# Performance work log

Hardware: AMD Instinct MI355X
Metric: run time of the kernel (lower is better)

## Reference

```python
import jax, jax.numpy as jnp
import numpy as np

PATCH = 64
STRIDE = PATCH // 2
SEQ = 65536
NPATCH = (SEQ - PATCH) // STRIDE + 1  # 2047
B = 256
EPS = 1e-5


def setup_inputs() -> dict:
    key = jax.random.key(0)
    ks = jax.random.split(key, 10)
    s = lambda k, shp: jax.random.normal(k, shp, jnp.float32) * 0.05
    return dict(
        x=jax.random.normal(ks[0], (B, 1, SEQ), jnp.float32),
        conv1_w=s(ks[1], (NPATCH, NPATCH - 1)),
        conv1_b=s(ks[2], (NPATCH,)),
        w1=s(ks[3], (32, 3, 5)), b1=s(ks[4], (32,)),
        g1=jnp.ones((32,), jnp.float32), be1=jnp.zeros((32,), jnp.float32),
        w2=s(ks[5], (64, 32, 3)), b2=s(ks[6], (64,)),
        g2=jnp.ones((64,), jnp.float32), be2=jnp.zeros((64,), jnp.float32),
        w3=s(ks[7], (128, 64, 3)), b3=s(ks[8], (128,)),
        g3=jnp.ones((128,), jnp.float32), be3=jnp.zeros((128,), jnp.float32),
    )


def _conv1d(x, w, b, pad):
    # x: [B, Cin, L], w: [Cout, Cin, K]
    y = jax.lax.conv_general_dilated(x, w, (1,), [(pad, pad)],
                                     dimension_numbers=('NCH', 'OIH', 'NCH'))
    return y + b[None, :, None]


def _bn(x, g, be):
    # training-mode BatchNorm1d: biased var over (batch, length)
    m = jnp.mean(x, axis=(0, 2), keepdims=True)
    v = jnp.var(x, axis=(0, 2), keepdims=True)
    return (x - m) * jax.lax.rsqrt(v + EPS) * g[None, :, None] + be[None, :, None]


def _maxpool2(x):
    # MaxPool1d(kernel=2, stride=2), floor division of length
    L = x.shape[-1] // 2
    return x[..., : 2 * L].reshape(x.shape[0], x.shape[1], L, 2).max(-1)


def reference(x, conv1_w, conv1_b, w1, b1, g1, be1, w2, b2, g2, be2, w3, b3, g3, be3):
    starts = jnp.arange(NPATCH) * STRIDE
    idx = starts[:, None] + jnp.arange(PATCH)[None, :]         # [NW, W]
    xp = x[:, :, idx]                                          # [B,1,NW,W]
    mean = xp.mean(-1)                                         # [B,1,NW]
    std = jnp.std(xp, axis=-1, ddof=1)                         # torch.std is unbiased
    stats = jnp.concatenate([mean, std], axis=1)               # [B,2,NW]
    dx = jnp.diff(xp, axis=2)                                  # diff across window index: [B,1,NW-1,W]
    dmax = dx.max(-1)                                          # [B,1,NW-1]
    dmax = jnp.transpose(dmax, (0, 2, 1))                      # [B,NW-1,1]
    # conv1: 1x1 Conv1d over length-1 axis == matmul over channel dim
    d2 = jnp.einsum('oi,bil->bol', conv1_w, dmax) + conv1_b[None, :, None]  # [B,NW,1]
    d2 = jnp.transpose(d2, (0, 2, 1))                          # [B,1,NW]
    x3 = jnp.concatenate([stats, d2], axis=1)                  # [B,3,NW]
    h = _maxpool2(jax.nn.relu(_bn(_conv1d(x3, w1, b1, 2), g1, be1)))
    h = _maxpool2(jax.nn.relu(_bn(_conv1d(h, w2, b2, 1), g2, be2)))
    h = jax.nn.relu(_bn(_conv1d(h, w3, b3, 1), g3, be3))
    return h.mean(-1)                                          # AdaptiveAvgPool1d(1)+Flatten -> [B,128]
```

## Files before the change

### kernel.cpp

```cpp
#include <hip/hip_runtime.h>
#include <math.h>

#define NB 256
#define SEQ 65536
#define NP 2047
#define NPM 2046
#define NPP 2048
#define KPAD 2048
#define LEN1 2047
#define LEN2 1023
#define LEN3 511
#define C1 32
#define C2 64
#define C3 128
#define NPART 2048
#define NPART2 (NB*4)
#define LPAD 514
#define SROW 40

#define OFF_X3   0
#define SZ_X3    (NB*3*NPP)
#define OFF_DMAX (OFF_X3 + SZ_X3)
#define SZ_DMAX  (NB*NPM)
#define OFF_Y1   (OFF_DMAX + SZ_DMAX)
#define SZ_Y1    (NB*C1*LEN1)
#define OFF_Y2   (OFF_Y1 + SZ_Y1)
#define SZ_Y2    (NB*C2*LEN2)
#define OFF_S1   (OFF_Y2 + SZ_Y2)
#define OFF_S2   (OFF_S1 + 2*C1)
#define OFF_S3   (OFF_S2 + 2*C2)
#define OFF_W2C  (OFF_S3 + 2*C3)
#define OFF_W3B  (OFF_W2C + C1*C2*3)
#define OFF_PS   (OFF_W3B + C2*C3*3)
#define OFF_PQ   (OFF_PS + C3*NPART)
#define OFF_WB   OFF_Y2
#define OFF_H1R  OFF_Y2
#define OFF_H2T  OFF_Y2
#define OFF_PM   (OFF_Y1 + 4300000)
#define OFF_W2B  OFF_W2C

typedef __attribute__((ext_vector_type(8))) short short8;
typedef __attribute__((ext_vector_type(4))) short short4v;
typedef __attribute__((ext_vector_type(4))) float f32x4;

__device__ inline short f2bf(float f){
  union { float f; unsigned u; } x; x.f = f;
  unsigned r = x.u + 0x7FFF + ((x.u >> 16) & 1);
  return (short)(r >> 16);
}

#define RED4L(v) v += __shfl_xor(v,1,64); v += __shfl_xor(v,2,64); \
                 v += __shfl_xor(v,4,64); v += __shfl_xor(v,8,64);

#define TILES(X) X(0,0) X(0,1) X(0,2) X(0,3) X(1,0) X(1,1) X(1,2) X(1,3) \
                 X(2,0) X(2,1) X(2,2) X(2,3) X(3,0) X(3,1) X(3,2) X(3,3)
#define DECLBIAS(P,ct) f32x4 bi##ct = *(const f32x4*)((P) + cbase + ct*16 + kq*4);
#define DECLACC(lt,ct) f32x4 acc##lt##ct = bi##ct;

__global__ __launch_bounds__(256) void k_patch(const float* __restrict__ x, const float* __restrict__ c1b,
                                               float* __restrict__ ws){
  float* x3    = ws + OFF_X3;
  short* dmaxB = (short*)(ws + OFF_DMAX);
  int b = blockIdx.y;
  int chunk = blockIdx.x;
  const float* xr = x + (size_t)b*SEQ + chunk*2048;
  __shared__ float Ss[65], Qs[65], Dm[65];
  int w = threadIdx.x >> 6;
  int l = threadIdx.x & 63;
  #pragma unroll
  for (int i=0;i<2;i++){
    int seg = w*2 + i;
    int off = seg*256;
    float4 A = *(const float4*)(xr + off + l*4);
    float4 Bh = make_float4(0.f,0.f,0.f,0.f);
    if (l >= 56){
      int g = chunk*2048 + off + 256 + (l-56)*4;
      if (g + 3 < SEQ) Bh = *(const float4*)(xr + off + 256 + (l-56)*4);
    }
    int src = (l+8) & 63;
    float p0 = __shfl(A.x, src, 64), p1 = __shfl(A.y, src, 64),
          p2 = __shfl(A.z, src, 64), p3 = __shfl(A.w, src, 64);
    if (l >= 56){ p0=Bh.x; p1=Bh.y; p2=Bh.z; p3=Bh.w; }
    float s = (A.x+A.y)+(A.z+A.w);
    float q = fmaf(A.x,A.x, fmaf(A.y,A.y, fmaf(A.z,A.z, A.w*A.w)));
    float d = fmaxf(fmaxf(p0-A.x, p1-A.y), fmaxf(p2-A.z, p3-A.w));
    #pragma unroll
    for (int o=1;o<8;o<<=1){
      s += __shfl_xor(s,o,64);
      q += __shfl_xor(q,o,64);
      d  = fmaxf(d, __shfl_xor(d,o,64));
    }
    if ((l&7)==0){ int m = seg*8 + (l>>3); Ss[m]=s; Qs[m]=q; Dm[m]=d; }
  }
  if (w==0){
    float s=0.f,q=0.f,d=-1e30f;
    if (l < 8){
      int g = chunk*2048 + 2048 + l*4;
      if (g+3 < SEQ){
        float4 A = *(const float4*)(xr + 2048 + l*4);
        float4 P = make_float4(0.f,0.f,0.f,0.f);
        if (g+35 < SEQ) P = *(const float4*)(xr + 2048 + 32 + l*4);
        s = (A.x+A.y)+(A.z+A.w);
        q = fmaf(A.x,A.x, fmaf(A.y,A.y, fmaf(A.z,A.z, A.w*A.w)));
        d = fmaxf(fmaxf(P.x-A.x, P.y-A.y), fmaxf(P.z-A.z, P.w-A.w));
      }
    }
    #pragma unroll
    for (int o=1;o<8;o<<=1){
      s += __shfl_xor(s,o,64);
      q += __shfl_xor(q,o,64);
      d  = fmaxf(d, __shfl_xor(d,o,64));
    }
    if (l==0){ Ss[64]=s; Qs[64]=q; Dm[64]=d; }
  }
  __syncthreads();
  if (threadIdx.x < 64){
    int j = threadIdx.x;
    int p = chunk*64 + j;
    if (p < NP){
      float S = Ss[j]+Ss[j+1];
      float Q = Qs[j]+Qs[j+1];
      float mean = S*(1.0f/64.0f);
      float var  = (Q - S*mean)*(1.0f/63.0f);
      x3[(size_t)(b*3+0)*NPP + p] = mean;
      x3[(size_t)(b*3+1)*NPP + p] = sqrtf(fmaxf(var,0.0f));
      x3[(size_t)(b*3+2)*NPP + p] = c1b[p];
    }
    dmaxB[(size_t)b*KPAD + p] = (p < NPM) ? f2bf(fmaxf(Dm[j], Dm[j+1])) : (short)0;
  }
}

__global__ __launch_bounds__(256) void k_prep(const float* __restrict__ W, const float* __restrict__ w2,
                                              const float* __restrict__ w3, float* __restrict__ ws){
  int bid = blockIdx.x;
  if (bid < 8*NP){
    short* Wb = (short*)(ws + OFF_WB);
    int o = bid >> 3;
    int k = (bid & 7)*256 + threadIdx.x;
    Wb[(size_t)o*KPAD + k] = (k < NPM) ? f2bf(W[(size_t)o*NPM + k]) : (short)0;
  } else {
    short* w2b = (short*)(ws + OFF_W2B);
    short* w3b = (short*)(ws + OFF_W3B);
    int t = (bid - 8*NP)*256 + threadIdx.x;
    if (t < 3*C2*C1){
      int tap = t / (C2*C1);
      int r = t - tap*(C2*C1);
      int c = r >> 5, i = r & 31;
      w2b[t] = f2bf(w2[(c*C1 + i)*3 + tap]);
    }
    if (t < 3*C3*C2){
      int tap = t / (C3*C2);
      int r = t - tap*(C3*C2);
      int c = r / C2, i = r - c*C2;
      w3b[(tap*C3 + c)*C2 + i] = f2bf(w3[(c*C2+i)*3 + tap]);
    }
  }
}

__global__ __launch_bounds__(256) void k_gemm(float* __restrict__ ws){
  const short* Ab = (const short*)(ws + OFF_DMAX);
  const short* Bb = (const short*)(ws + OFF_WB);
  float* x3 = ws + OFF_X3;
  int wid  = __builtin_amdgcn_readfirstlane(threadIdx.x >> 6);
  int lane = threadIdx.x & 63;
  int ln = lane & 15, kq = lane >> 4;
  int n0  = blockIdx.x*32;
  int m16 = (blockIdx.y*4 + wid)*16;
  int ks  = blockIdx.z*512;
  f32x4 acc0 = {0.f,0.f,0.f,0.f}, acc1 = {0.f,0.f,0.f,0.f};
  int o0 = n0 + ln, o1 = n0 + 16 + ln;
  const short* ap  = Ab + (size_t)(m16 + ln)*KPAD + ks + kq*8;
  const short* bp0 = Bb + (size_t)min(o0, NP-1)*KPAD + ks + kq*8;
  const short* bp1 = Bb + (size_t)min(o1, NP-1)*KPAD + ks + kq*8;
  #pragma unroll 4
  for (int s=0; s<16; s++){
    short8 av = *(const short8*)(ap  + s*32);
    short8 b0 = *(const short8*)(bp0 + s*32);
    short8 b1 = *(const short8*)(bp1 + s*32);
    acc0 = __builtin_amdgcn_mfma_f32_16x16x32_bf16(av, b0, acc0, 0, 0, 0);
    acc1 = __builtin_amdgcn_mfma_f32_16x16x32_bf16(av, b1, acc1, 0, 0, 0);
  }
  #pragma unroll
  for (int r=0;r<4;r++){
    int b = m16 + kq*4 + r;
    float* xp = x3 + ((size_t)(b*3) + 2)*NPP;
    if (o0 < NP) atomicAdd(xp + o0, acc0[r]);
    if (o1 < NP) atomicAdd(xp + o1, acc1[r]);
  }
}

__global__ __launch_bounds__(256) void k_conv1f(const float* __restrict__ w1, const float* __restrict__ b1, float* __restrict__ ws){
  const float* x3 = ws + OFF_X3;
  float* h1r = ws + OFF_H1R;
  float* ps = ws + OFF_PS;
  float* pq = ws + OFF_PQ;
  int b = blockIdx.y;
  int blk = blockIdx.x;
  int w = threadIdx.x >> 6;
  int lane = threadIdx.x & 63;
  int h = lane >> 5, c = lane & 31;
  int p0 = blk*256 + w*64 + h*32;
  float wv[3][5];
  #pragma unroll
  for (int i=0;i<3;i++){
    #pragma unroll
    for (int j=0;j<5;j++) wv[i][j] = w1[(c*3+i)*5+j];
  }
  float bc = b1[c];
  const float* xb = x3 + (size_t)b*3*NPP;
  float s = 0.f, q = 0.f;
  #pragma unroll
  for (int k0=0;k0<32;k0+=8){
    int base = p0 + k0 - 4;
    float xw[3][16];
    #pragma unroll
    for (int i=0;i<3;i++){
      const float* xr = xb + (size_t)i*NPP;
      if (base >= 0 && base + 16 <= LEN1){
        #pragma unroll
        for (int t=0;t<4;t++) *(f32x4*)&xw[i][4*t] = *(const f32x4*)(xr + base + 4*t);
      } else {
        #pragma unroll
        for (int t=0;t<16;t++){ int g = base + t; xw[i][t] = (g >= 0 && g < LEN1) ? xr[g] : 0.f; }
      }
    }
    float acc[8];
    #pragma unroll
    for (int k=0;k<8;k++){
      float a = bc;
      #pragma unroll
      for (int i=0;i<3;i++){
        #pragma unroll
        for (int j=0;j<5;j++) a = fmaf(wv[i][j], xw[i][k+j+2], a);
      }
      acc[k] = a;
      if (p0 + k0 + k < LEN1){ s += a; q = fmaf(a, a, q); }
    }
    #pragma unroll
    for (int t=0;t<4;t++){
      int m = ((p0 + k0) >> 1) + t;
      if (m < LEN2) h1r[((size_t)b*LEN2 + m)*C1 + c] = fmaxf(acc[2*t], acc[2*t+1]);
    }
  }
  s += __shfl_xor(s, 32, 64);
  q += __shfl_xor(q, 32, 64);
  __shared__ float es[4][C1], eq[4][C1];
  if (h == 0){ es[w][c] = s; eq[w][c] = q; }
  __syncthreads();
  if (threadIdx.x < C1){
    int cc = threadIdx.x;
    float S = es[0][cc]+es[1][cc]+es[2][cc]+es[3][cc];
    float Q = eq[0][cc]+eq[1][cc]+eq[2][cc]+eq[3][cc];
    ps[(size_t)cc*NPART + b*8 + blk] = S;
    pq[(size_t)cc*NPART + b*8 + blk] = Q;
  }
}

__global__ __launch_bounds__(256) void k_fin(const float* __restrict__ ps, const float* __restrict__ pq,
                                             const float* __restrict__ g, const float* __restrict__ be,
                                             float* __restrict__ stats, int C, int npart, double invN,
                                             float* __restrict__ outz){
  if (outz) outz[(size_t)threadIdx.x * C3 + blockIdx.x] = 0.f;
  int c = blockIdx.x;
  double s=0.0, q=0.0;
  for (int j=threadIdx.x; j<npart; j+=256){ s += (double)ps[c*npart+j]; q += (double)pq[c*npart+j]; }
  #pragma unroll
  for (int off=32; off; off>>=1){ s += __shfl_xor(s,off,64); q += __shfl_xor(q,off,64); }
  __shared__ double rs[4], rq[4];
  int wid = threadIdx.x>>6, lane=threadIdx.x&63;
  if (lane==0){ rs[wid]=s; rq[wid]=q; }
  __syncthreads();
  if (threadIdx.x==0){
    double S = rs[0]+rs[1]+rs[2]+rs[3];
    double Q = rq[0]+rq[1]+rq[2]+rq[3];
    double mean = S*invN;
    double var  = Q*invN - mean*mean;
    double a = (double)g[c] / sqrt(var + 1e-5);
    stats[c]   = (float)a;
    stats[C+c] = (float)((double)be[c] - mean*a);
  }
}

__global__ __launch_bounds__(256) void k_conv2m(const float* __restrict__ b2, float* __restrict__ ws){
  const float* h1r = ws + OFF_H1R;
  const float* st1 = ws + OFF_S1;
  const short* w2b = (const short*)(ws + OFF_W2B);
  float* pmaxT = ws + OFF_PM;
  float* ps = ws + OFF_PS;
  float* pq = ws + OFF_PQ;
  int b   = blockIdx.y;
  int blk = blockIdx.x;
  int l0  = blk*256;
  __shared__ __align__(16) short sh[258*SROW];
  for (int u = threadIdx.x; u < 258*8; u += 256){
    int row = u >> 3, g = u & 7;
    int pos = l0 - 1 + row;
    short4v r4 = (short4v)0;
    if (pos >= 0 && pos < LEN2){
      f32x4 xv = *(const f32x4*)(h1r + ((size_t)b*LEN2 + pos)*C1 + g*4);
      f32x4 av = *(const f32x4*)(st1 + g*4);
      f32x4 bb = *(const f32x4*)(st1 + C1 + g*4);
      #pragma unroll
      for (int j=0;j<4;j++) r4[j] = f2bf(fmaxf(fmaf(av[j], xv[j], bb[j]), 0.f));
    }
    *(short4v*)(sh + row*SROW + g*4) = r4;
  }
  __syncthreads();
  int w   = __builtin_amdgcn_readfirstlane(threadIdx.x >> 6);
  int lane = threadIdx.x & 63;
  int ln = lane & 15, kq = lane >> 4;
  int lw = l0 + w*64;
  int cbase = 0;
  DECLBIAS(b2,0) DECLBIAS(b2,1) DECLBIAS(b2,2) DECLBIAS(b2,3)
  TILES(DECLACC)
  const short* wA = w2b + (size_t)ln*C1 + kq*8;
#define LDW(T,ct) short8 aw##T##ct = *(const short8*)(wA + (size_t)(T*C2 + ct*16)*C1);
  LDW(0,0) LDW(0,1) LDW(0,2) LDW(0,3)
  LDW(1,0) LDW(1,1) LDW(1,2) LDW(1,3)
  LDW(2,0) LDW(2,1) LDW(2,2) LDW(2,3)
#undef LDW
#define MMT0(lt,ct) acc##lt##ct = __builtin_amdgcn_mfma_f32_16x16x32_bf16(aw0##ct, bv##lt, acc##lt##ct, 0, 0, 0);
#define MMT1(lt,ct) acc##lt##ct = __builtin_amdgcn_mfma_f32_16x16x32_bf16(aw1##ct, bv##lt, acc##lt##ct, 0, 0, 0);
#define MMT2(lt,ct) acc##lt##ct = __builtin_amdgcn_mfma_f32_16x16x32_bf16(aw2##ct, bv##lt, acc##lt##ct, 0, 0, 0);
#define LDB2(lt,T) short8 bv##lt = *(const short8*)(sh + (size_t)(w*64 + lt*16 + T + ln)*SROW + kq*8);
#define CSTEP(T) { LDB2(0,T) LDB2(1,T) LDB2(2,T) LDB2(3,T) TILES(MMT##T) }
  CSTEP(0) CSTEP(1) CSTEP(2)
#undef CSTEP
#undef LDB2
#define PST(lt,ct) { \
    float p0_ = fmaxf(acc##lt##ct[0], __shfl_xor(acc##lt##ct[0],1,64)); \
    float p1_ = fmaxf(acc##lt##ct[1], __shfl_xor(acc##lt##ct[1],1,64)); \
    float p2_ = fmaxf(acc##lt##ct[2], __shfl_xor(acc##lt##ct[2],1,64)); \
    float p3_ = fmaxf(acc##lt##ct[3], __shfl_xor(acc##lt##ct[3],1,64)); \
    int l_ = lw + lt*16 + ln; \
    if (!(ln & 1) && (l_ >> 1) < LEN3){ \
      f32x4 pv_ = {p0_, p1_, p2_, p3_}; \
      *(f32x4*)(pmaxT + ((size_t)b*LEN3 + (l_>>1))*C2 + ct*16 + kq*4) = pv_; } }
  TILES(PST)
#undef PST
  __shared__ float es[4][C2], eq[4][C2];
  #pragma unroll
  for (int ct=0;ct<4;ct++){
    float s0=0.f,s1=0.f,s2=0.f,s3=0.f,q0=0.f,q1=0.f,q2=0.f,q3=0.f;
#define ACCST(lt,CT) if (CT == ct){ int l_ = lw + lt*16 + ln; if (l_ < LEN2){ \
      s0 += acc##lt##CT[0]; q0 = fmaf(acc##lt##CT[0], acc##lt##CT[0], q0); \
      s1 += acc##lt##CT[1]; q1 = fmaf(acc##lt##CT[1], acc##lt##CT[1], q1); \
      s2 += acc##lt##CT[2]; q2 = fmaf(acc##lt##CT[2], acc##lt##CT[2], q2); \
      s3 += acc##lt##CT[3]; q3 = fmaf(acc##lt##CT[3], acc##lt##CT[3], q3); } }
    TILES(ACCST)
#undef ACCST
    RED4L(s0) RED4L(s1) RED4L(s2) RED4L(s3)
    RED4L(q0) RED4L(q1) RED4L(q2) RED4L(q3)
    if (ln == 0){
      int c0 = ct*16 + kq*4;
      es[w][c0+0]=s0; es[w][c0+1]=s1; es[w][c0+2]=s2; es[w][c0+3]=s3;
      eq[w][c0+0]=q0; eq[w][c0+1]=q1; eq[w][c0+2]=q2; eq[w][c0+3]=q3;
    }
  }
  __syncthreads();
  if (threadIdx.x < C2){
    int c = threadIdx.x;
    float S = es[0][c]+es[1][c]+es[2][c]+es[3][c];
    float Q = eq[0][c]+eq[1][c]+eq[2][c]+eq[3][c];
    ps[(size_t)c*NPART2 + b*4 + blk] = S;
    pq[(size_t)c*NPART2 + b*4 + blk] = Q;
  }
}

__global__ __launch_bounds__(256) void k_p2bf(float* __restrict__ ws){
  const float* pm = ws + OFF_PM;
  const float* st = ws + OFF_S2;
  short* h2t = (short*)(ws + OFF_H2T);
  int b = blockIdx.y;
  int idx = blockIdx.x*256 + threadIdx.x;
  if (idx < LEN3*C2){
    int m = idx >> 6, c = idx & 63;
    float v = fmaxf(fmaf(st[c], pm[((size_t)b*LEN3 + m)*C2 + c], st[C2+c]), 0.f);
    h2t[(((size_t)b*8 + (c>>3))*LPAD + m + 1)*8 + (c&7)] = f2bf(v);
  } else {
    int zr = idx - LEN3*C2;
    if (zr < 3*C2){
      int rsel = zr >> 6, c = zr & 63;
      int row = (rsel == 0) ? 0 : (511 + rsel);
      h2t[(((size_t)b*8 + (c>>3))*LPAD + row)*8 + (c&7)] = 0;
    }
  }
}

__global__ __launch_bounds__(256) void k_conv3s(const float* __restrict__ b3, float* __restrict__ ws){
  const short* h2t = (const short*)(ws + OFF_H2T);
  const short* w3b = (const short*)(ws + OFF_W3B);
  float* ps = ws + OFF_PS;
  float* pq = ws + OFF_PQ;
  int b   = blockIdx.y;
  int blk = blockIdx.x;
  int wid = __builtin_amdgcn_readfirstlane(threadIdx.x >> 6);
  int lane = threadIdx.x & 63;
  int ln = lane & 15, kq = lane >> 4;
  int lh = wid & 1, ch = wid >> 1;
  int l0 = blk*128 + lh*64;
  int cbase = ch*64;
  DECLBIAS(b3,0) DECLBIAS(b3,1) DECLBIAS(b3,2) DECLBIAS(b3,3)
  TILES(DECLACC)
  const short* hB = h2t + (((size_t)b*8 + kq)*LPAD + l0 + ln)*8;
  const short* wA = w3b + (size_t)(cbase + ln)*C2 + kq*8;
  #pragma unroll
  for (int t=0;t<3;t++){
    #pragma unroll
    for (int s=0;s<2;s++){
#define LDB(lt) short8 bv##lt = *(const short8*)(hB + ((size_t)s*4*LPAD + lt*16 + t)*8);
      LDB(0) LDB(1) LDB(2) LDB(3)
#define LDA(ct) short8 av##ct = *(const short8*)(wA + (size_t)(t*C3 + ct*16)*C2 + s*32);
      LDA(0) LDA(1) LDA(2) LDA(3)
#define MM(lt,ct) acc##lt##ct = __builtin_amdgcn_mfma_f32_16x16x32_bf16(av##ct, bv##lt, acc##lt##ct, 0, 0, 0);
      TILES(MM)
#undef LDB
#undef LDA
    }
  }
  int pidx = b*8 + blk*2 + lh;
  #pragma unroll
  for (int ct=0;ct<4;ct++){
    float s0=0.f,s1=0.f,s2=0.f,s3=0.f,q0=0.f,q1=0.f,q2=0.f,q3=0.f;
#define ACCST(lt,CT) if (CT == ct){ int l_ = l0 + lt*16 + ln; if (l_ < LEN3){ \
      s0 += acc##lt##CT[0]; q0 = fmaf(acc##lt##CT[0], acc##lt##CT[0], q0); \
      s1 += acc##lt##CT[1]; q1 = fmaf(acc##lt##CT[1], acc##lt##CT[1], q1); \
      s2 += acc##lt##CT[2]; q2 = fmaf(acc##lt##CT[2], acc##lt##CT[2], q2); \
      s3 += acc##lt##CT[3]; q3 = fmaf(acc##lt##CT[3], acc##lt##CT[3], q3); } }
    TILES(ACCST)
#undef ACCST
    RED4L(s0) RED4L(s1) RED4L(s2) RED4L(s3)
    RED4L(q0) RED4L(q1) RED4L(q2) RED4L(q3)
    if (ln == 0){
      int c0 = cbase + ct*16 + kq*4;
      ps[(size_t)(c0+0)*NPART + pidx] = s0;  pq[(size_t)(c0+0)*NPART + pidx] = q0;
      ps[(size_t)(c0+1)*NPART + pidx] = s1;  pq[(size_t)(c0+1)*NPART + pidx] = q1;
      ps[(size_t)(c0+2)*NPART + pidx] = s2;  pq[(size_t)(c0+2)*NPART + pidx] = q2;
      ps[(size_t)(c0+3)*NPART + pidx] = s3;  pq[(size_t)(c0+3)*NPART + pidx] = q3;
    }
  }
}

__global__ __launch_bounds__(256) void k_out3(float* __restrict__ out, const float* __restrict__ b3,
                                              const float* __restrict__ ws){
  const short* h2t = (const short*)(ws + OFF_H2T);
  const short* w3b = (const short*)(ws + OFF_W3B);
  const float* st  = ws + OFF_S3;
  int b   = blockIdx.y;
  int blk = blockIdx.x;
  int wid = __builtin_amdgcn_readfirstlane(threadIdx.x >> 6);
  int lane = threadIdx.x & 63;
  int ln = lane & 15, kq = lane >> 4;
  int lh = wid & 1, ch = wid >> 1;
  int l0 = blk*128 + lh*64;
  int cbase = ch*64;
  DECLBIAS(b3,0) DECLBIAS(b3,1) DECLBIAS(b3,2) DECLBIAS(b3,3)
  TILES(DECLACC)
  const short* hB = h2t + (((size_t)b*8 + kq)*LPAD + l0 + ln)*8;
  const short* wA = w3b + (size_t)(cbase + ln)*C2 + kq*8;
  #pragma unroll
  for (int t=0;t<3;t++){
    #pragma unroll
    for (int s=0;s<2;s++){
#define LDB(lt) short8 bv##lt = *(const short8*)(hB + ((size_t)s*4*LPAD + lt*16 + t)*8);
      LDB(0) LDB(1) LDB(2) LDB(3)
#define LDA(ct) short8 av##ct = *(const short8*)(wA + (size_t)(t*C3 + ct*16)*C2 + s*32);
      LDA(0) LDA(1) LDA(2) LDA(3)
      TILES(MM)
#undef LDB
#undef LDA
    }
  }
  const float inv = 1.0f/511.0f;
  #pragma unroll
  for (int ct=0;ct<4;ct++){
    int c0 = cbase + ct*16 + kq*4;
    float a0 = st[c0+0], a1 = st[c0+1], a2 = st[c0+2], a3 = st[c0+3];
    float h0 = st[C3+c0+0], h1_ = st[C3+c0+1], h2_ = st[C3+c0+2], h3 = st[C3+c0+3];
    float s0=0.f,s1=0.f,s2=0.f,s3=0.f;
#define OSUM(lt,CT) if (CT == ct){ int l_ = l0 + lt*16 + ln; if (l_ < LEN3){ \
      s0 += fmaxf(fmaf(a0, acc##lt##CT[0], h0 ), 0.f); \
      s1 += fmaxf(fmaf(a1, acc##lt##CT[1], h1_), 0.f); \
      s2 += fmaxf(fmaf(a2, acc##lt##CT[2], h2_), 0.f); \
      s3 += fmaxf(fmaf(a3, acc##lt##CT[3], h3 ), 0.f); } }
    TILES(OSUM)
#undef OSUM
    RED4L(s0) RED4L(s1) RED4L(s2) RED4L(s3)
    if (ln == 0){
      atomicAdd(out + (size_t)b*C3 + c0+0, s0*inv);
      atomicAdd(out + (size_t)b*C3 + c0+1, s1*inv);
      atomicAdd(out + (size_t)b*C3 + c0+2, s2*inv);
      atomicAdd(out + (size_t)b*C3 + c0+3, s3*inv);
    }
  }
}

extern "C" void kernel_launch(void* const* d_in, const int* in_sizes, int n_in,
                              void* d_out, int out_size, void* d_ws, size_t ws_size,
                              hipStream_t stream) {
  const float* x   = (const float*)d_in[0];
  const float* c1w = (const float*)d_in[1];
  const float* c1b = (const float*)d_in[2];
  const float* w1  = (const float*)d_in[3];
  const float* b1  = (const float*)d_in[4];
  const float* g1  = (const float*)d_in[5];
  const float* be1 = (const float*)d_in[6];
  const float* w2  = (const float*)d_in[7];
  const float* b2  = (const float*)d_in[8];
  const float* g2  = (const float*)d_in[9];
  const float* be2 = (const float*)d_in[10];
  const float* w3  = (const float*)d_in[11];
  const float* b3  = (const float*)d_in[12];
  const float* g3  = (const float*)d_in[13];
  const float* be3 = (const float*)d_in[14];
  float* ws  = (float*)d_ws;
  float* out = (float*)d_out;

  hipLaunchKernelGGL(k_patch,  dim3(32,NB), dim3(256), 0, stream, x, c1b, ws);
  hipLaunchKernelGGL(k_prep,   dim3(8*NP + 96), dim3(256), 0, stream, c1w, w2, w3, ws);
  hipLaunchKernelGGL(k_gemm,   dim3(64,4,4), dim3(256), 0, stream, ws);
  hipLaunchKernelGGL(k_conv1f, dim3(8,NB), dim3(256), 0, stream, w1, b1, ws);
  hipLaunchKernelGGL(k_fin,    dim3(C1), dim3(256), 0, stream, ws+OFF_PS, ws+OFF_PQ, g1, be1, ws+OFF_S1, C1, NPART, 1.0/((double)NB*LEN1), (float*)nullptr);
  hipLaunchKernelGGL(k_conv2m, dim3(4,NB), dim3(256), 0, stream, b2, ws);
  hipLaunchKernelGGL(k_fin,    dim3(C2), dim3(256), 0, stream, ws+OFF_PS, ws+OFF_PQ, g2, be2, ws+OFF_S2, C2, NPART2, 1.0/((double)NB*LEN2), (float*)nullptr);
  hipLaunchKernelGGL(k_p2bf,   dim3((LEN3*C2+3*C2+255)/256, NB), dim3(256), 0, stream, ws);
  hipLaunchKernelGGL(k_conv3s, dim3(4,NB), dim3(256), 0, stream, b3, ws);
  hipLaunchKernelGGL(k_fin,    dim3(C3), dim3(256), 0, stream, ws+OFF_PS, ws+OFF_PQ, g3, be3, ws+OFF_S3, C3, NPART, 1.0/((double)NB*LEN3), out);
  hipLaunchKernelGGL(k_out3,   dim3(4,NB), dim3(256), 0, stream, out, b3, ws);
}
```

Measured before the change: 289.2 us.

## Fuse patch/prep kernels, drop p2bf pass, stage conv3 input in LDS, widen gemm tiles

Merges the patch-statistics and weight-prep kernels into one launch. Conv2's pooled output is now stored as bf16 instead of fp32. The separate BN2+ReLU+bf16 transpose kernel is removed; conv3s and out3 each apply BN2 and ReLU while staging a haloed input tile into shared memory. The gemm now has each block cover all 256 batch rows with four accumulator tiles, dropping the batch grid dimension. This cuts launches and intermediate global traffic, and reduces the number of blocks that re-read the W matrix. In exchange the BN2 normalisation is recomputed in two kernels, and the gemm grid shrinks to 256 blocks.

```diff
diff --git a/kernel.cpp b/kernel.cpp
--- a/kernel.cpp
+++ b/kernel.cpp
@@ -15,8 +15,8 @@
 #define C3 128
 #define NPART 2048
 #define NPART2 (NB*4)
-#define LPAD 514
 #define SROW 40
+#define SROW3 72
 
 #define OFF_X3   0
 #define SZ_X3    (NB*3*NPP)
@@ -35,7 +35,6 @@
 #define OFF_PQ   (OFF_PS + C3*NPART)
 #define OFF_WB   OFF_Y2
 #define OFF_H1R  OFF_Y2
-#define OFF_H2T  OFF_Y2
 #define OFF_PM   (OFF_Y1 + 4300000)
 #define OFF_W2B  OFF_W2C
 
@@ -48,6 +47,9 @@
   unsigned r = x.u + 0x7FFF + ((x.u >> 16) & 1);
   return (short)(r >> 16);
 }
+__device__ inline float bf2f(short s){
+  union { unsigned u; float f; } x; x.u = ((unsigned)(unsigned short)s) << 16; return x.f;
+}
 
 #define RED4L(v) v += __shfl_xor(v,1,64); v += __shfl_xor(v,2,64); \
                  v += __shfl_xor(v,4,64); v += __shfl_xor(v,8,64);
@@ -57,102 +59,103 @@
 #define DECLBIAS(P,ct) f32x4 bi##ct = *(const f32x4*)((P) + cbase + ct*16 + kq*4);
 #define DECLACC(lt,ct) f32x4 acc##lt##ct = bi##ct;
 
-__global__ __launch_bounds__(256) void k_patch(const float* __restrict__ x, const float* __restrict__ c1b,
-                                               float* __restrict__ ws){
-  float* x3    = ws + OFF_X3;
-  short* dmaxB = (short*)(ws + OFF_DMAX);
-  int b = blockIdx.y;
-  int chunk = blockIdx.x;
-  const float* xr = x + (size_t)b*SEQ + chunk*2048;
-  __shared__ float Ss[65], Qs[65], Dm[65];
-  int w = threadIdx.x >> 6;
-  int l = threadIdx.x & 63;
-  #pragma unroll
-  for (int i=0;i<2;i++){
-    int seg = w*2 + i;
-    int off = seg*256;
-    float4 A = *(const float4*)(xr + off + l*4);
-    float4 Bh = make_float4(0.f,0.f,0.f,0.f);
-    if (l >= 56){
-      int g = chunk*2048 + off + 256 + (l-56)*4;
-      if (g + 3 < SEQ) Bh = *(const float4*)(xr + off + 256 + (l-56)*4);
-    }
-    int src = (l+8) & 63;
-    float p0 = __shfl(A.x, src, 64), p1 = __shfl(A.y, src, 64),
-          p2 = __shfl(A.z, src, 64), p3 = __shfl(A.w, src, 64);
-    if (l >= 56){ p0=Bh.x; p1=Bh.y; p2=Bh.z; p3=Bh.w; }
-    float s = (A.x+A.y)+(A.z+A.w);
-    float q = fmaf(A.x,A.x, fmaf(A.y,A.y, fmaf(A.z,A.z, A.w*A.w)));
-    float d = fmaxf(fmaxf(p0-A.x, p1-A.y), fmaxf(p2-A.z, p3-A.w));
-    #pragma unroll
-    for (int o=1;o<8;o<<=1){
-      s += __shfl_xor(s,o,64);
-      q += __shfl_xor(q,o,64);
-      d  = fmaxf(d, __shfl_xor(d,o,64));
-    }
-    if ((l&7)==0){ int m = seg*8 + (l>>3); Ss[m]=s; Qs[m]=q; Dm[m]=d; }
-  }
-  if (w==0){
-    float s=0.f,q=0.f,d=-1e30f;
-    if (l < 8){
-      int g = chunk*2048 + 2048 + l*4;
-      if (g+3 < SEQ){
-        float4 A = *(const float4*)(xr + 2048 + l*4);
-        float4 P = make_float4(0.f,0.f,0.f,0.f);
-        if (g+35 < SEQ) P = *(const float4*)(xr + 2048 + 32 + l*4);
-        s = (A.x+A.y)+(A.z+A.w);
-        q = fmaf(A.x,A.x, fmaf(A.y,A.y, fmaf(A.z,A.z, A.w*A.w)));
-        d = fmaxf(fmaxf(P.x-A.x, P.y-A.y), fmaxf(P.z-A.z, P.w-A.w));
-      }
-    }
-    #pragma unroll
-    for (int o=1;o<8;o<<=1){
-      s += __shfl_xor(s,o,64);
-      q += __shfl_xor(q,o,64);
-      d  = fmaxf(d, __shfl_xor(d,o,64));
-    }
-    if (l==0){ Ss[64]=s; Qs[64]=q; Dm[64]=d; }
-  }
-  __syncthreads();
-  if (threadIdx.x < 64){
-    int j = threadIdx.x;
-    int p = chunk*64 + j;
-    if (p < NP){
-      float S = Ss[j]+Ss[j+1];
-      float Q = Qs[j]+Qs[j+1];
-      float mean = S*(1.0f/64.0f);
-      float var  = (Q - S*mean)*(1.0f/63.0f);
-      x3[(size_t)(b*3+0)*NPP + p] = mean;
-      x3[(size_t)(b*3+1)*NPP + p] = sqrtf(fmaxf(var,0.0f));
-      x3[(size_t)(b*3+2)*NPP + p] = c1b[p];
-    }
-    dmaxB[(size_t)b*KPAD + p] = (p < NPM) ? f2bf(fmaxf(Dm[j], Dm[j+1])) : (short)0;
-  }
-}
-
-__global__ __launch_bounds__(256) void k_prep(const float* __restrict__ W, const float* __restrict__ w2,
-                                              const float* __restrict__ w3, float* __restrict__ ws){
+__global__ __launch_bounds__(256) void k_pp(const float* __restrict__ x, const float* __restrict__ c1b,
+                                            const float* __restrict__ W, const float* __restrict__ w2,
+                                            const float* __restrict__ w3, float* __restrict__ ws){
   int bid = blockIdx.x;
-  if (bid < 8*NP){
-    short* Wb = (short*)(ws + OFF_WB);
-    int o = bid >> 3;
-    int k = (bid & 7)*256 + threadIdx.x;
-    Wb[(size_t)o*KPAD + k] = (k < NPM) ? f2bf(W[(size_t)o*NPM + k]) : (short)0;
+  if (bid < 32*NB){
+    float* x3    = ws + OFF_X3;
+    short* dmaxB = (short*)(ws + OFF_DMAX);
+    int b = bid >> 5;
+    int chunk = bid & 31;
+    const float* xr = x + (size_t)b*SEQ + chunk*2048;
+    __shared__ float Ss[65], Qs[65], Dm[65];
+    int w = threadIdx.x >> 6;
+    int l = threadIdx.x & 63;
+    #pragma unroll
+    for (int i=0;i<2;i++){
+      int seg = w*2 + i;
+      int off = seg*256;
+      float4 A = *(const float4*)(xr + off + l*4);
+      float4 Bh = make_float4(0.f,0.f,0.f,0.f);
+      if (l >= 56){
+        int g = chunk*2048 + off + 256 + (l-56)*4;
+        if (g + 3 < SEQ) Bh = *(const float4*)(xr + off + 256 + (l-56)*4);
+      }
+      int src = (l+8) & 63;
+      float p0 = __shfl(A.x, src, 64), p1 = __shfl(A.y, src, 64),
+            p2 = __shfl(A.z, src, 64), p3 = __shfl(A.w, src, 64);
+      if (l >= 56){ p0=Bh.x; p1=Bh.y; p2=Bh.z; p3=Bh.w; }
+      float s = (A.x+A.y)+(A.z+A.w);
+      float q = fmaf(A.x,A.x, fmaf(A.y,A.y, fmaf(A.z,A.z, A.w*A.w)));
+      float d = fmaxf(fmaxf(p0-A.x, p1-A.y), fmaxf(p2-A.z, p3-A.w));
+      #pragma unroll
+      for (int o=1;o<8;o<<=1){
+        s += __shfl_xor(s,o,64);
+        q += __shfl_xor(q,o,64);
+        d  = fmaxf(d, __shfl_xor(d,o,64));
+      }
+      if ((l&7)==0){ int m = seg*8 + (l>>3); Ss[m]=s; Qs[m]=q; Dm[m]=d; }
+    }
+    if (w==0){
+      float s=0.f,q=0.f,d=-1e30f;
+      if (l < 8){
+        int g = chunk*2048 + 2048 + l*4;
+        if (g+3 < SEQ){
+          float4 A = *(const float4*)(xr + 2048 + l*4);
+          float4 P = make_float4(0.f,0.f,0.f,0.f);
+          if (g+35 < SEQ) P = *(const float4*)(xr + 2048 + 32 + l*4);
+          s = (A.x+A.y)+(A.z+A.w);
+          q = fmaf(A.x,A.x, fmaf(A.y,A.y, fmaf(A.z,A.z, A.w*A.w)));
+          d = fmaxf(fmaxf(P.x-A.x, P.y-A.y), fmaxf(P.z-A.z, P.w-A.w));
+        }
+      }
+      #pragma unroll
+      for (int o=1;o<8;o<<=1){
+        s += __shfl_xor(s,o,64);
+        q += __shfl_xor(q,o,64);
+        d  = fmaxf(d, __shfl_xor(d,o,64));
+      }
+      if (l==0){ Ss[64]=s; Qs[64]=q; Dm[64]=d; }
+    }
+    __syncthreads();
+    if (threadIdx.x < 64){
+      int j = threadIdx.x;
+      int p = chunk*64 + j;
+      if (p < NP){
+        float S = Ss[j]+Ss[j+1];
+        float Q = Qs[j]+Qs[j+1];
+        float mean = S*(1.0f/64.0f);
+        float var  = (Q - S*mean)*(1.0f/63.0f);
+        x3[(size_t)(b*3+0)*NPP + p] = mean;
+        x3[(size_t)(b*3+1)*NPP + p] = sqrtf(fmaxf(var,0.0f));
+        x3[(size_t)(b*3+2)*NPP + p] = c1b[p];
+      }
+      dmaxB[(size_t)b*KPAD + p] = (p < NPM) ? f2bf(fmaxf(Dm[j], Dm[j+1])) : (short)0;
+    }
   } else {
-    short* w2b = (short*)(ws + OFF_W2B);
-    short* w3b = (short*)(ws + OFF_W3B);
-    int t = (bid - 8*NP)*256 + threadIdx.x;
-    if (t < 3*C2*C1){
-      int tap = t / (C2*C1);
-      int r = t - tap*(C2*C1);
-      int c = r >> 5, i = r & 31;
-      w2b[t] = f2bf(w2[(c*C1 + i)*3 + tap]);
-    }
-    if (t < 3*C3*C2){
-      int tap = t / (C3*C2);
-      int r = t - tap*(C3*C2);
-      int c = r / C2, i = r - c*C2;
-      w3b[(tap*C3 + c)*C2 + i] = f2bf(w3[(c*C2+i)*3 + tap]);
+    int pb = bid - 32*NB;
+    if (pb < 8*NP){
+      short* Wb = (short*)(ws + OFF_WB);
+      int o = pb >> 3;
+      int k = (pb & 7)*256 + threadIdx.x;
+      Wb[(size_t)o*KPAD + k] = (k < NPM) ? f2bf(W[(size_t)o*NPM + k]) : (short)0;
+    } else {
+      short* w2b = (short*)(ws + OFF_W2B);
+      short* w3b = (short*)(ws + OFF_W3B);
+      int t = (pb - 8*NP)*256 + threadIdx.x;
+      if (t < 3*C2*C1){
+        int tap = t / (C2*C1);
+        int r = t - tap*(C2*C1);
+        int c = r >> 5, i = r & 31;
+        w2b[t] = f2bf(w2[(c*C1 + i)*3 + tap]);
+      }
+      if (t < 3*C3*C2){
+        int tap = t / (C3*C2);
+        int r = t - tap*(C3*C2);
+        int c = r / C2, i = r - c*C2;
+        w3b[(tap*C3 + c)*C2 + i] = f2bf(w3[(c*C2+i)*3 + tap]);
+      }
     }
   }
 }
@@ -165,27 +168,34 @@
   int lane = threadIdx.x & 63;
   int ln = lane & 15, kq = lane >> 4;
   int n0  = blockIdx.x*32;
-  int m16 = (blockIdx.y*4 + wid)*16;
-  int ks  = blockIdx.z*512;
-  f32x4 acc0 = {0.f,0.f,0.f,0.f}, acc1 = {0.f,0.f,0.f,0.f};
+  int ks  = blockIdx.y*512;
+  f32x4 acc[4][2];
+  #pragma unroll
+  for (int bt=0;bt<4;bt++){ acc[bt][0] = (f32x4){0.f,0.f,0.f,0.f}; acc[bt][1] = (f32x4){0.f,0.f,0.f,0.f}; }
   int o0 = n0 + ln, o1 = n0 + 16 + ln;
-  const short* ap  = Ab + (size_t)(m16 + ln)*KPAD + ks + kq*8;
+  const short* ap  = Ab + (size_t)(wid*16 + ln)*KPAD + ks + kq*8;
   const short* bp0 = Bb + (size_t)min(o0, NP-1)*KPAD + ks + kq*8;
   const short* bp1 = Bb + (size_t)min(o1, NP-1)*KPAD + ks + kq*8;
-  #pragma unroll 4
+  #pragma unroll 2
   for (int s=0; s<16; s++){
-    short8 av = *(const short8*)(ap  + s*32);
     short8 b0 = *(const short8*)(bp0 + s*32);
     short8 b1 = *(const short8*)(bp1 + s*32);
-    acc0 = __builtin_amdgcn_mfma_f32_16x16x32_bf16(av, b0, acc0, 0, 0, 0);
-    acc1 = __builtin_amdgcn_mfma_f32_16x16x32_bf16(av, b1, acc1, 0, 0, 0);
-  }
-  #pragma unroll
-  for (int r=0;r<4;r++){
-    int b = m16 + kq*4 + r;
-    float* xp = x3 + ((size_t)(b*3) + 2)*NPP;
-    if (o0 < NP) atomicAdd(xp + o0, acc0[r]);
-    if (o1 < NP) atomicAdd(xp + o1, acc1[r]);
+    #pragma unroll
+    for (int bt=0;bt<4;bt++){
+      short8 av = *(const short8*)(ap + (size_t)bt*64*KPAD + s*32);
+      acc[bt][0] = __builtin_amdgcn_mfma_f32_16x16x32_bf16(av, b0, acc[bt][0], 0, 0, 0);
+      acc[bt][1] = __builtin_amdgcn_mfma_f32_16x16x32_bf16(av, b1, acc[bt][1], 0, 0, 0);
+    }
+  }
+  #pragma unroll
+  for (int bt=0;bt<4;bt++){
+    #pragma unroll
+    for (int r=0;r<4;r++){
+      int b = bt*64 + wid*16 + kq*4 + r;
+      float* xp = x3 + ((size_t)(b*3) + 2)*NPP;
+      if (o0 < NP) atomicAdd(xp + o0, acc[bt][0][r]);
+      if (o1 < NP) atomicAdd(xp + o1, acc[bt][1][r]);
+    }
   }
 }
 
@@ -285,7 +295,7 @@
   const float* h1r = ws + OFF_H1R;
   const float* st1 = ws + OFF_S1;
   const short* w2b = (const short*)(ws + OFF_W2B);
-  float* pmaxT = ws + OFF_PM;
+  short* pmB = (short*)(ws + OFF_PM);
   float* ps = ws + OFF_PS;
   float* pq = ws + OFF_PQ;
   int b   = blockIdx.y;
@@ -334,8 +344,8 @@
     float p3_ = fmaxf(acc##lt##ct[3], __shfl_xor(acc##lt##ct[3],1,64)); \
     int l_ = lw + lt*16 + ln; \
     if (!(ln & 1) && (l_ >> 1) < LEN3){ \
-      f32x4 pv_ = {p0_, p1_, p2_, p3_}; \
-      *(f32x4*)(pmaxT + ((size_t)b*LEN3 + (l_>>1))*C2 + ct*16 + kq*4) = pv_; } }
+      short4v pv_ = { f2bf(p0_), f2bf(p1_), f2bf(p2_), f2bf(p3_) }; \
+      *(short4v*)(pmB + ((size_t)b*LEN3 + (l_>>1))*C2 + ct*16 + kq*4) = pv_; } }
   TILES(PST)
 #undef PST
   __shared__ float es[4][C2], eq[4][C2];
@@ -367,48 +377,51 @@
   }
 }
 
-__global__ __launch_bounds__(256) void k_p2bf(float* __restrict__ ws){
-  const float* pm = ws + OFF_PM;
-  const float* st = ws + OFF_S2;
-  short* h2t = (short*)(ws + OFF_H2T);
-  int b = blockIdx.y;
-  int idx = blockIdx.x*256 + threadIdx.x;
-  if (idx < LEN3*C2){
-    int m = idx >> 6, c = idx & 63;
-    float v = fmaxf(fmaf(st[c], pm[((size_t)b*LEN3 + m)*C2 + c], st[C2+c]), 0.f);
-    h2t[(((size_t)b*8 + (c>>3))*LPAD + m + 1)*8 + (c&7)] = f2bf(v);
-  } else {
-    int zr = idx - LEN3*C2;
-    if (zr < 3*C2){
-      int rsel = zr >> 6, c = zr & 63;
-      int row = (rsel == 0) ? 0 : (511 + rsel);
-      h2t[(((size_t)b*8 + (c>>3))*LPAD + row)*8 + (c&7)] = 0;
-    }
-  }
-}
+#define STAGE3(SH, BB, L0BLK) \
+  for (int u = threadIdx.x; u < 130*8; u += 256){ \
+    int row_ = u >> 3, g_ = u & 7; \
+    int pos_ = (L0BLK) - 1 + row_; \
+    short8 r8_ = (short8)0; \
+    if (pos_ >= 0 && pos_ < LEN3){ \
+      short8 xm_ = *(const short8*)(pmB + ((size_t)(BB)*LEN3 + pos_)*C2 + g_*8); \
+      f32x4 alo_ = *(const f32x4*)(st2 + g_*8),      ahi_ = *(const f32x4*)(st2 + g_*8 + 4); \
+      f32x4 blo_ = *(const f32x4*)(st2 + C2 + g_*8), bhi_ = *(const f32x4*)(st2 + C2 + g_*8 + 4); \
+      _Pragma("unroll") \
+      for (int j=0;j<4;j++){ \
+        r8_[j]   = f2bf(fmaxf(fmaf(alo_[j], bf2f(xm_[j]),   blo_[j]), 0.f)); \
+        r8_[j+4] = f2bf(fmaxf(fmaf(ahi_[j], bf2f(xm_[j+4]), bhi_[j]), 0.f)); \
+      } \
+    } \
+    *(short8*)(SH + (size_t)row_*SROW3 + g_*8) = r8_; \
+  }
 
 __global__ __launch_bounds__(256) void k_conv3s(const float* __restrict__ b3, float* __restrict__ ws){
-  const short* h2t = (const short*)(ws + OFF_H2T);
+  const short* pmB = (const short*)(ws + OFF_PM);
+  const float* st2 = ws + OFF_S2;
   const short* w3b = (const short*)(ws + OFF_W3B);
   float* ps = ws + OFF_PS;
   float* pq = ws + OFF_PQ;
   int b   = blockIdx.y;
   int blk = blockIdx.x;
+  int l0blk = blk*128;
+  __shared__ __align__(16) short sh[130*SROW3];
+  STAGE3(sh, b, l0blk)
+  __syncthreads();
   int wid = __builtin_amdgcn_readfirstlane(threadIdx.x >> 6);
   int lane = threadIdx.x & 63;
   int ln = lane & 15, kq = lane >> 4;
   int lh = wid & 1, ch = wid >> 1;
-  int l0 = blk*128 + lh*64;
+  int l0 = l0blk + lh*64;
   int cbase = ch*64;
   DECLBIAS(b3,0) DECLBIAS(b3,1) DECLBIAS(b3,2) DECLBIAS(b3,3)
   TILES(DECLACC)
-  const short* hB = h2t + (((size_t)b*8 + kq)*LPAD + l0 + ln)*8;
+  const short* hL = sh + (size_t)(lh*64 + ln)*SROW3 + kq*8;
   const short* wA = w3b + (size_t)(cbase + ln)*C2 + kq*8;
   #pragma unroll
   for (int t=0;t<3;t++){
     #pragma unroll
     for (int s=0;s<2;s++){
-#define LDB(lt) short8 bv##lt = *(const short8*)(hB + ((size_t)s*4*LPAD + lt*16 + t)*8);
+#define LDB(lt) short8 bv##lt = *(const short8*)(hL + (size_t)(lt*16 + t)*SROW3 + s*32);
       LDB(0) LDB(1) LDB(2) LDB(3)
 #define LDA(ct) short8 av##ct = *(const short8*)(wA + (size_t)(t*C3 + ct*16)*C2 + s*32);
       LDA(0) LDA(1) LDA(2) LDA(3)
@@ -443,26 +456,31 @@
 
 __global__ __launch_bounds__(256) void k_out3(float* __restrict__ out, const float* __restrict__ b3,
                                               const float* __restrict__ ws){
-  const short* h2t = (const short*)(ws + OFF_H2T);
+  const short* pmB = (const short*)(ws + OFF_PM);
+  const float* st2 = ws + OFF_S2;
   const short* w3b = (const short*)(ws + OFF_W3B);
   const float* st  = ws + OFF_S3;
   int b   = blockIdx.y;
   int blk = blockIdx.x;
+  int l0blk = blk*128;
+  __shared__ __align__(16) short sh[130*SROW3];
+  STAGE3(sh, b, l0blk)
+  __syncthreads();
   int wid = __builtin_amdgcn_readfirstlane(threadIdx.x >> 6);
   int lane = threadIdx.x & 63;
   int ln = lane & 15, kq = lane >> 4;
   int lh = wid & 1, ch = wid >> 1;
-  int l0 = blk*128 + lh*64;
+  int l0 = l0blk + lh*64;
   int cbase = ch*64;
   DECLBIAS(b3,0) DECLBIAS(b3,1) DECLBIAS(b3,2) DECLBIAS(b3,3)
   TILES(DECLACC)
-  const short* hB = h2t + (((size_t)b*8 + kq)*LPAD + l0 + ln)*8;
+  const short* hL = sh + (size_t)(lh*64 + ln)*SROW3 + kq*8;
   const short* wA = w3b + (size_t)(cbase + ln)*C2 + kq*8;
   #pragma unroll
   for (int t=0;t<3;t++){
     #pragma unroll
     for (int s=0;s<2;s++){
-#define LDB(lt) short8 bv##lt = *(const short8*)(hB + ((size_t)s*4*LPAD + lt*16 + t)*8);
+#define LDB(lt) short8 bv##lt = *(const short8*)(hL + (size_t)(lt*16 + t)*SROW3 + s*32);
       LDB(0) LDB(1) LDB(2) LDB(3)
 #define LDA(ct) short8 av##ct = *(const short8*)(wA + (size_t)(t*C3 + ct*16)*C2 + s*32);
       LDA(0) LDA(1) LDA(2) LDA(3)
@@ -516,14 +534,12 @@
   float* ws  = (float*)d_ws;
   float* out = (float*)d_out;
 
-  hipLaunchKernelGGL(k_patch,  dim3(32,NB), dim3(256), 0, stream, x, c1b, ws);
-  hipLaunchKernelGGL(k_prep,   dim3(8*NP + 96), dim3(256), 0, stream, c1w, w2, w3, ws);
-  hipLaunchKernelGGL(k_gemm,   dim3(64,4,4), dim3(256), 0, stream, ws);
+  hipLaunchKernelGGL(k_pp,     dim3(32*NB + 8*NP + 96), dim3(256), 0, stream, x, c1b, c1w, w2, w3, ws);
+  hipLaunchKernelGGL(k_gemm,   dim3(64,4), dim3(256), 0, stream, ws);
   hipLaunchKernelGGL(k_conv1f, dim3(8,NB), dim3(256), 0, stream, w1, b1, ws);
   hipLaunchKernelGGL(k_fin,    dim3(C1), dim3(256), 0, stream, ws+OFF_PS, ws+OFF_PQ, g1, be1, ws+OFF_S1, C1, NPART, 1.0/((double)NB*LEN1), (float*)nullptr);
   hipLaunchKernelGGL(k_conv2m, dim3(4,NB), dim3(256), 0, stream, b2, ws);
   hipLaunchKernelGGL(k_fin,    dim3(C2), dim3(256), 0, stream, ws+OFF_PS, ws+OFF_PQ, g2, be2, ws+OFF_S2, C2, NPART2, 1.0/((double)NB*LEN2), (float*)nullptr);
-  hipLaunchKernelGGL(k_p2bf,   dim3((LEN3*C2+3*C2+255)/256, NB), dim3(256), 0, stream, ws);
   hipLaunchKernelGGL(k_conv3s, dim3(4,NB), dim3(256), 0, stream, b3, ws);
   hipLaunchKernelGGL(k_fin,    dim3(C3), dim3(256), 0, stream, ws+OFF_PS, ws+OFF_PQ, g3, be3, ws+OFF_S3, C3, NPART, 1.0/((double)NB*LEN3), out);
   hipLaunchKernelGGL(k_out3,   dim3(4,NB), dim3(256), 0, stream, out, b3, ws);
```

Result: faster. 263.1 us (-9.0%).
